# Kernel optimization log

Hardware: AMD Instinct MI355X
Metric: run time of the kernel (lower is better)

## Reference

```python
import jax, jax.numpy as jnp
import numpy as np
from jax import lax

KERNEL = 3
STRIDE = 1
PADDING = 1
DILATION = 1


def setup_inputs() -> dict:
    key = jax.random.key(0)
    k1, k2, k3, k4, k5 = jax.random.split(key, 5)
    B, C, H, W = 8, 64, 256, 256
    x = jax.random.normal(k1, (B, C, H, W), dtype=jnp.float32)
    depthwise_weights = jax.random.normal(k2, (C, 1, KERNEL, KERNEL), dtype=jnp.float32)
    pointwise_weights = jax.random.normal(k3, (C, C, 1, 1), dtype=jnp.float32)
    attention_weights = jax.random.normal(k4, (C, C), dtype=jnp.float32)
    global_attention_weight = jax.random.normal(k5, (C, C), dtype=jnp.float32)
    return {
        "x": x,
        "depthwise_weights": depthwise_weights,
        "pointwise_weights": pointwise_weights,
        "attention_weights": attention_weights,
        "global_attention_weight": global_attention_weight,
    }


def reference(x, depthwise_weights, pointwise_weights, attention_weights, global_attention_weight):
    C = x.shape[1]
    # Depthwise conv: groups == C, NCHW / OIHW layout.
    dw = lax.conv_general_dilated(
        x,
        depthwise_weights,
        window_strides=(STRIDE, STRIDE),
        padding=[(PADDING, PADDING), (PADDING, PADDING)],
        rhs_dilation=(DILATION, DILATION),
        feature_group_count=C,
        dimension_numbers=("NCHW", "OIHW", "NCHW"),
    )  # [B, C, Ho, Wo]
    # Per-pixel channel attention (row-softmax over mixing matrix).
    A = jax.nn.softmax(attention_weights, axis=1)  # [C, C]
    att = jnp.einsum("cd,bdhw->bchw", A, dw)
    # 1x1 pointwise conv (channel mix).
    pw = jnp.einsum("kc,bchw->bkhw", pointwise_weights[:, :, 0, 0], att)
    # Global channel attention.
    G = jax.nn.softmax(global_attention_weight, axis=1)  # [C, C]
    out = jnp.einsum("cd,bdhw->bchw", G, pw)
    return out
```

## Files before the change

kernel.cpp:

```cpp
#include <hip/hip_runtime.h>
#include <math.h>

#define HH 256
#define WW 256
#define CC 64
#define NB 8
#define ROWS 8

typedef float fvec4 __attribute__((ext_vector_type(4)));

__global__ __launch_bounds__(1024) void prep_M(const float* __restrict__ A,
                                               const float* __restrict__ G,
                                               const float* __restrict__ P,
                                               float* __restrict__ Mt) {
    __shared__ __align__(16) float As[64][68];
    __shared__ __align__(16) float Gs[64][68];
    __shared__ __align__(16) float T[64][68];

    const int t = threadIdx.x;
    const int wave = t >> 6;
    const int lane = t & 63;

    for (int r8 = 0; r8 < 8; ++r8) {
        int row = wave * 8 + r8;
        int r = row & 63;
        const float* src = (row < 64) ? A : G;
        float v = src[r * 64 + lane];
        float m = v;
        #pragma unroll
        for (int off = 32; off > 0; off >>= 1)
            m = fmaxf(m, __shfl_xor(m, off, 64));
        float e = __expf(v - m);
        float s = e;
        #pragma unroll
        for (int off = 32; off > 0; off >>= 1)
            s += __shfl_xor(s, off, 64);
        float o = e / s;
        if (row < 64) As[r][lane] = o; else Gs[r][lane] = o;
    }
    __syncthreads();

    {
        const int d = t >> 4, q = t & 15;
        float4 acc = make_float4(0.f, 0.f, 0.f, 0.f);
        for (int e = 0; e < 64; ++e) {
            float p = P[d * 64 + e];
            float4 a = *(const float4*)&As[e][4 * q];
            acc.x = fmaf(p, a.x, acc.x);
            acc.y = fmaf(p, a.y, acc.y);
            acc.z = fmaf(p, a.z, acc.z);
            acc.w = fmaf(p, a.w, acc.w);
        }
        *(float4*)&T[d][4 * q] = acc;
    }
    __syncthreads();

    {
        const int k = t >> 4, q = t & 15;
        float4 acc = make_float4(0.f, 0.f, 0.f, 0.f);
        for (int d = 0; d < 64; ++d) {
            float g = Gs[k][d];
            float4 tv = *(const float4*)&T[d][4 * q];
            acc.x = fmaf(g, tv.x, acc.x);
            acc.y = fmaf(g, tv.y, acc.y);
            acc.z = fmaf(g, tv.z, acc.z);
            acc.w = fmaf(g, tv.w, acc.w);
        }
        Mt[(4 * q + 0) * 64 + k] = acc.x;
        Mt[(4 * q + 1) * 64 + k] = acc.y;
        Mt[(4 * q + 2) * 64 + k] = acc.z;
        Mt[(4 * q + 3) * 64 + k] = acc.w;
    }
}

__global__ __launch_bounds__(256, 3) void fused_conv_mix(const float* __restrict__ x,
                                                         const float* __restrict__ dwgt,
                                                         const float* __restrict__ Mt,
                                                         float* __restrict__ out) {
    __shared__ __align__(16) float MtS[64][64];
    __shared__ __align__(16) float dwS[2][64][68];

    const int t = threadIdx.x;
    const int tw0 = blockIdx.x * 64;
    const int h0 = blockIdx.y * ROWS;
    const int b = blockIdx.z;

    {
        const float4* m4 = (const float4*)Mt;
        float4* s4 = (float4*)&MtS[0][0];
        #pragma unroll
        for (int j = 0; j < 4; ++j) s4[j * 256 + t] = m4[j * 256 + t];
    }

    const int c = t >> 2;
    const int chunk = t & 3;
    const int gw0 = tw0 + chunk * 16;
    const float* xc = x + ((size_t)(b * CC + c) * HH) * WW;

    float wg[9];
    #pragma unroll
    for (int i = 0; i < 9; ++i) wg[i] = dwgt[c * 9 + i];

    float rm[18], r0[18], rp[18], rn[18];

    auto load_row = [&](float* r, int y) {
        if ((unsigned)y < (unsigned)HH) {
            const float* p = xc + y * WW + gw0;
            const float4* p4 = (const float4*)p;
            float4 v0 = p4[0], v1 = p4[1], v2 = p4[2], v3 = p4[3];
            r[1] = v0.x;  r[2] = v0.y;  r[3] = v0.z;  r[4] = v0.w;
            r[5] = v1.x;  r[6] = v1.y;  r[7] = v1.z;  r[8] = v1.w;
            r[9] = v2.x;  r[10] = v2.y; r[11] = v2.z; r[12] = v2.w;
            r[13] = v3.x; r[14] = v3.y; r[15] = v3.z; r[16] = v3.w;
            r[0]  = (gw0 > 0)       ? p[-1] : 0.f;
            r[17] = (gw0 + 16 < WW) ? p[16] : 0.f;
        } else {
            #pragma unroll
            for (int i = 0; i < 18; ++i) r[i] = 0.f;
        }
    };

    load_row(rm, h0 - 1);
    load_row(r0, h0);
    load_row(rp, h0 + 1);

    __syncthreads();

    const int ki = t >> 4;
    const int wj = t & 15;
    const size_t kstride = (size_t)HH * WW;

    #pragma unroll 1
    for (int i = 0; i < ROWS; ++i) {
        {
            #pragma unroll
            for (int v = 0; v < 4; ++v) {
                float4 o4;
                float* oo = (float*)&o4;
                #pragma unroll
                for (int u = 0; u < 4; ++u) {
                    int j = 4 * v + u;
                    float a = 0.f;
                    #pragma unroll
                    for (int dx = 0; dx < 3; ++dx) {
                        a = fmaf(wg[0 * 3 + dx], rm[j + dx], a);
                        a = fmaf(wg[1 * 3 + dx], r0[j + dx], a);
                        a = fmaf(wg[2 * 3 + dx], rp[j + dx], a);
                    }
                    oo[u] = a;
                }
                *(float4*)&dwS[i & 1][c][chunk * 16 + 4 * v] = o4;
            }
        }
        __syncthreads();

        if (i < ROWS - 1) load_row(rn, h0 + i + 2);

        {
            float o00 = 0.f, o01 = 0.f, o02 = 0.f, o03 = 0.f;
            float o10 = 0.f, o11 = 0.f, o12 = 0.f, o13 = 0.f;
            float o20 = 0.f, o21 = 0.f, o22 = 0.f, o23 = 0.f;
            float o30 = 0.f, o31 = 0.f, o32 = 0.f, o33 = 0.f;

            #pragma unroll 4
            for (int cc2 = 0; cc2 < 64; ++cc2) {
                float4 m = *(const float4*)&MtS[cc2][4 * ki];
                float4 d = *(const float4*)&dwS[i & 1][cc2][4 * wj];
                o00 = fmaf(m.x, d.x, o00); o01 = fmaf(m.x, d.y, o01);
                o02 = fmaf(m.x, d.z, o02); o03 = fmaf(m.x, d.w, o03);
                o10 = fmaf(m.y, d.x, o10); o11 = fmaf(m.y, d.y, o11);
                o12 = fmaf(m.y, d.z, o12); o13 = fmaf(m.y, d.w, o13);
                o20 = fmaf(m.z, d.x, o20); o21 = fmaf(m.z, d.y, o21);
                o22 = fmaf(m.z, d.z, o22); o23 = fmaf(m.z, d.w, o23);
                o30 = fmaf(m.w, d.x, o30); o31 = fmaf(m.w, d.y, o31);
                o32 = fmaf(m.w, d.z, o32); o33 = fmaf(m.w, d.w, o33);
            }

            float* ob = out + ((size_t)(b * CC) * HH + (h0 + i)) * WW + tw0 + 4 * wj;
            const int k = 4 * ki;
            fvec4 s0 = {o00, o01, o02, o03};
            fvec4 s1 = {o10, o11, o12, o13};
            fvec4 s2 = {o20, o21, o22, o23};
            fvec4 s3 = {o30, o31, o32, o33};
            __builtin_nontemporal_store(s0, (fvec4*)(ob + (size_t)(k + 0) * kstride));
            __builtin_nontemporal_store(s1, (fvec4*)(ob + (size_t)(k + 1) * kstride));
            __builtin_nontemporal_store(s2, (fvec4*)(ob + (size_t)(k + 2) * kstride));
            __builtin_nontemporal_store(s3, (fvec4*)(ob + (size_t)(k + 3) * kstride));
        }

        #pragma unroll
        for (int j = 0; j < 18; ++j) { rm[j] = r0[j]; r0[j] = rp[j]; rp[j] = rn[j]; }
    }
}

extern "C" void kernel_launch(void* const* d_in, const int* in_sizes, int n_in,
                              void* d_out, int out_size, void* d_ws, size_t ws_size,
                              hipStream_t stream) {
    const float* x    = (const float*)d_in[0];
    const float* dwgt = (const float*)d_in[1];
    const float* pwgt = (const float*)d_in[2];
    const float* attw = (const float*)d_in[3];
    const float* gatt = (const float*)d_in[4];
    float* Mt = (float*)d_ws;
    float* o  = (float*)d_out;

    prep_M<<<1, 1024, 0, stream>>>(attw, gatt, pwgt, Mt);

    dim3 grid(WW / 64, HH / ROWS, NB);
    fused_conv_mix<<<grid, 256, 0, stream>>>(x, dwgt, Mt, o);
}
```

Measured before the change: 287.2 us.

## Use fp16 MFMA for channel mix with transposed depthwise tile

Replaces the scalar FP32 64x64 channel-mixing GEMM with MFMA 16x16x32 fp16 instructions. The combined mixing matrix is stored in fp16 by the prep kernel and loaded straight into registers instead of shared memory. The depthwise tile is now stored transposed, the row ring buffer is rotated by full unrolling instead of copying, and occupancy is raised to 4 blocks per SM. Converting activations to fp16 reduces precision, and the output stores become scalar rather than float4.

```diff
diff --git a/kernel.cpp b/kernel.cpp
--- a/kernel.cpp
+++ b/kernel.cpp
@@ -8,11 +8,13 @@
 #define ROWS 8
 
 typedef float fvec4 __attribute__((ext_vector_type(4)));
+typedef float floatx4 __attribute__((ext_vector_type(4)));
+typedef _Float16 half8 __attribute__((ext_vector_type(8)));
 
 __global__ __launch_bounds__(1024) void prep_M(const float* __restrict__ A,
                                                const float* __restrict__ G,
                                                const float* __restrict__ P,
-                                               float* __restrict__ Mt) {
+                                               _Float16* __restrict__ Mh) {
     __shared__ __align__(16) float As[64][68];
     __shared__ __align__(16) float Gs[64][68];
     __shared__ __align__(16) float T[64][68];
@@ -66,32 +68,25 @@
             acc.z = fmaf(g, tv.z, acc.z);
             acc.w = fmaf(g, tv.w, acc.w);
         }
-        Mt[(4 * q + 0) * 64 + k] = acc.x;
-        Mt[(4 * q + 1) * 64 + k] = acc.y;
-        Mt[(4 * q + 2) * 64 + k] = acc.z;
-        Mt[(4 * q + 3) * 64 + k] = acc.w;
+        _Float16* mp = Mh + k * 64 + 4 * q;
+        mp[0] = (_Float16)acc.x;
+        mp[1] = (_Float16)acc.y;
+        mp[2] = (_Float16)acc.z;
+        mp[3] = (_Float16)acc.w;
     }
 }
 
-__global__ __launch_bounds__(256, 3) void fused_conv_mix(const float* __restrict__ x,
+__global__ __launch_bounds__(256, 4) void fused_conv_mix(const float* __restrict__ x,
                                                          const float* __restrict__ dwgt,
-                                                         const float* __restrict__ Mt,
+                                                         const _Float16* __restrict__ Mh,
                                                          float* __restrict__ out) {
-    __shared__ __align__(16) float MtS[64][64];
-    __shared__ __align__(16) float dwS[2][64][68];
+    __shared__ __align__(16) float dwT[2][64][68];
 
     const int t = threadIdx.x;
     const int tw0 = blockIdx.x * 64;
     const int h0 = blockIdx.y * ROWS;
     const int b = blockIdx.z;
 
-    {
-        const float4* m4 = (const float4*)Mt;
-        float4* s4 = (float4*)&MtS[0][0];
-        #pragma unroll
-        for (int j = 0; j < 4; ++j) s4[j * 256 + t] = m4[j * 256 + t];
-    }
-
     const int c = t >> 2;
     const int chunk = t & 3;
     const int gw0 = tw0 + chunk * 16;
@@ -101,7 +96,19 @@
     #pragma unroll
     for (int i = 0; i < 9; ++i) wg[i] = dwgt[c * 9 + i];
 
-    float rm[18], r0[18], rp[18], rn[18];
+    const int wave = t >> 6;
+    const int lane = t & 63;
+    const int q = lane >> 4;
+    const int mrow = lane & 15;
+
+    half8 af0, af1;
+    {
+        const half8* ap = (const half8*)(Mh + (wave * 16 + mrow) * 64);
+        af0 = ap[q];
+        af1 = ap[4 + q];
+    }
+
+    float rows[3][18];
 
     auto load_row = [&](float* r, int y) {
         if ((unsigned)y < (unsigned)HH) {
@@ -120,76 +127,66 @@
         }
     };
 
-    load_row(rm, h0 - 1);
-    load_row(r0, h0);
-    load_row(rp, h0 + 1);
-
-    __syncthreads();
-
-    const int ki = t >> 4;
-    const int wj = t & 15;
+    load_row(rows[0], h0 - 1);
+    load_row(rows[1], h0);
+    load_row(rows[2], h0 + 1);
+
     const size_t kstride = (size_t)HH * WW;
 
-    #pragma unroll 1
+    #pragma unroll
     for (int i = 0; i < ROWS; ++i) {
+        const float* rm_ = rows[(i + 0) % 3];
+        const float* r0_ = rows[(i + 1) % 3];
+        const float* rp_ = rows[(i + 2) % 3];
+
+        #pragma unroll
+        for (int j = 0; j < 16; ++j) {
+            float a = 0.f;
+            #pragma unroll
+            for (int dx = 0; dx < 3; ++dx) {
+                a = fmaf(wg[0 * 3 + dx], rm_[j + dx], a);
+                a = fmaf(wg[1 * 3 + dx], r0_[j + dx], a);
+                a = fmaf(wg[2 * 3 + dx], rp_[j + dx], a);
+            }
+            dwT[i & 1][chunk * 16 + j][c] = a;
+        }
+        __syncthreads();
+
+        if (i < ROWS - 1) load_row(rows[i % 3], h0 + i + 2);
+
         {
-            #pragma unroll
-            for (int v = 0; v < 4; ++v) {
-                float4 o4;
-                float* oo = (float*)&o4;
+            floatx4 dd[4];
+            #pragma unroll
+            for (int s = 0; s < 4; ++s) dd[s] = (floatx4){0.f, 0.f, 0.f, 0.f};
+
+            #pragma unroll
+            for (int sub = 0; sub < 4; ++sub) {
+                const float* bp = &dwT[i & 1][sub * 16 + mrow][q * 8];
+                fvec4 alo = *(const fvec4*)(bp);
+                fvec4 ahi = *(const fvec4*)(bp + 4);
+                fvec4 blo = *(const fvec4*)(bp + 32);
+                fvec4 bhi = *(const fvec4*)(bp + 36);
+                half8 hb0, hb1;
                 #pragma unroll
-                for (int u = 0; u < 4; ++u) {
-                    int j = 4 * v + u;
-                    float a = 0.f;
-                    #pragma unroll
-                    for (int dx = 0; dx < 3; ++dx) {
-                        a = fmaf(wg[0 * 3 + dx], rm[j + dx], a);
-                        a = fmaf(wg[1 * 3 + dx], r0[j + dx], a);
-                        a = fmaf(wg[2 * 3 + dx], rp[j + dx], a);
-                    }
-                    oo[u] = a;
+                for (int j = 0; j < 4; ++j) {
+                    hb0[j]     = (_Float16)alo[j];
+                    hb0[j + 4] = (_Float16)ahi[j];
+                    hb1[j]     = (_Float16)blo[j];
+                    hb1[j + 4] = (_Float16)bhi[j];
                 }
-                *(float4*)&dwS[i & 1][c][chunk * 16 + 4 * v] = o4;
+                dd[sub] = __builtin_amdgcn_mfma_f32_16x16x32_f16(af0, hb0, dd[sub], 0, 0, 0);
+                dd[sub] = __builtin_amdgcn_mfma_f32_16x16x32_f16(af1, hb1, dd[sub], 0, 0, 0);
             }
-        }
-        __syncthreads();
-
-        if (i < ROWS - 1) load_row(rn, h0 + i + 2);
-
-        {
-            float o00 = 0.f, o01 = 0.f, o02 = 0.f, o03 = 0.f;
-            float o10 = 0.f, o11 = 0.f, o12 = 0.f, o13 = 0.f;
-            float o20 = 0.f, o21 = 0.f, o22 = 0.f, o23 = 0.f;
-            float o30 = 0.f, o31 = 0.f, o32 = 0.f, o33 = 0.f;
-
-            #pragma unroll 4
-            for (int cc2 = 0; cc2 < 64; ++cc2) {
-                float4 m = *(const float4*)&MtS[cc2][4 * ki];
-                float4 d = *(const float4*)&dwS[i & 1][cc2][4 * wj];
-                o00 = fmaf(m.x, d.x, o00); o01 = fmaf(m.x, d.y, o01);
-                o02 = fmaf(m.x, d.z, o02); o03 = fmaf(m.x, d.w, o03);
-                o10 = fmaf(m.y, d.x, o10); o11 = fmaf(m.y, d.y, o11);
-                o12 = fmaf(m.y, d.z, o12); o13 = fmaf(m.y, d.w, o13);
-                o20 = fmaf(m.z, d.x, o20); o21 = fmaf(m.z, d.y, o21);
-                o22 = fmaf(m.z, d.z, o22); o23 = fmaf(m.z, d.w, o23);
-                o30 = fmaf(m.w, d.x, o30); o31 = fmaf(m.w, d.y, o31);
-                o32 = fmaf(m.w, d.z, o32); o33 = fmaf(m.w, d.w, o33);
+
+            float* obase = out + (((size_t)(b * CC + wave * 16 + q * 4)) * HH + (h0 + i)) * WW + tw0;
+            #pragma unroll
+            for (int r = 0; r < 4; ++r) {
+                float* orow = obase + (size_t)r * kstride + mrow;
+                #pragma unroll
+                for (int sub = 0; sub < 4; ++sub)
+                    __builtin_nontemporal_store(dd[sub][r], orow + sub * 16);
             }
-
-            float* ob = out + ((size_t)(b * CC) * HH + (h0 + i)) * WW + tw0 + 4 * wj;
-            const int k = 4 * ki;
-            fvec4 s0 = {o00, o01, o02, o03};
-            fvec4 s1 = {o10, o11, o12, o13};
-            fvec4 s2 = {o20, o21, o22, o23};
-            fvec4 s3 = {o30, o31, o32, o33};
-            __builtin_nontemporal_store(s0, (fvec4*)(ob + (size_t)(k + 0) * kstride));
-            __builtin_nontemporal_store(s1, (fvec4*)(ob + (size_t)(k + 1) * kstride));
-            __builtin_nontemporal_store(s2, (fvec4*)(ob + (size_t)(k + 2) * kstride));
-            __builtin_nontemporal_store(s3, (fvec4*)(ob + (size_t)(k + 3) * kstride));
-        }
-
-        #pragma unroll
-        for (int j = 0; j < 18; ++j) { rm[j] = r0[j]; r0[j] = rp[j]; rp[j] = rn[j]; }
+        }
     }
 }
 
@@ -201,11 +198,11 @@
     const float* pwgt = (const float*)d_in[2];
     const float* attw = (const float*)d_in[3];
     const float* gatt = (const float*)d_in[4];
-    float* Mt = (float*)d_ws;
+    _Float16* Mh = (_Float16*)d_ws;
     float* o  = (float*)d_out;
 
-    prep_M<<<1, 1024, 0, stream>>>(attw, gatt, pwgt, Mt);
+    prep_M<<<1, 1024, 0, stream>>>(attw, gatt, pwgt, Mh);
 
     dim3 grid(WW / 64, HH / ROWS, NB);
-    fused_conv_mix<<<grid, 256, 0, stream>>>(x, dwgt, Mt, o);
+    fused_conv_mix<<<grid, 256, 0, stream>>>(x, dwgt, Mh, o);
 }
```

After: 257.8 us. 10.2% less time.
